# Performance work log

Measured on AMD Instinct MI355X. Metric: run time of the kernel, lower is better.

The kernel has to match this reference:

```python
import jax, jax.numpy as jnp
import numpy as np

N_NODES = 50000
N_EDGES = 800000
D_IN = 128
D_OUT = 128
K = 3


def setup_inputs() -> dict:
    key = jax.random.key(0)
    k1, k2, k3, k4 = jax.random.split(key, 4)
    x = jax.random.normal(k1, (N_NODES, D_IN), dtype=jnp.float32)
    src = jax.random.randint(k2, (N_EDGES,), 0, N_NODES, dtype=jnp.int32)
    dst = jax.random.randint(k3, (N_EDGES,), 0, N_NODES, dtype=jnp.int32)
    edge_index = jnp.stack([src, dst], axis=0)  # [2, E]
    W = jax.random.normal(k4, (D_OUT, D_IN * (K + 1)), dtype=jnp.float32) * 0.02
    b = jnp.zeros((D_OUT,), dtype=jnp.float32)
    return {"x": x, "edge_index": edge_index, "W": W, "b": b}


def _mean_propagate(h, src, dst, n_nodes):
    # scatter-mean: out[v] = mean_{(u,v) in E} h[u]
    msgs = h[src]                                             # [E, D] gather
    summed = jax.ops.segment_sum(msgs, dst, num_segments=n_nodes)
    cnt = jax.ops.segment_sum(jnp.ones((src.shape[0], 1), h.dtype), dst,
                              num_segments=n_nodes)
    return summed / jnp.maximum(cnt, 1.0)


def reference(x, edge_index, W, b):
    src, dst = edge_index[0], edge_index[1]
    n = x.shape[0]
    terms = [x]
    terms.append(_mean_propagate(x, src, dst, n))             # T1 = P x
    for _ in range(K - 1):                                    # T_k = 2 P T_{k-1} - T_{k-2}
        terms.append(2.0 * _mean_propagate(terms[-1], src, dst, n) - terms[-2])
    h = jnp.concatenate(terms, axis=-1)                       # [N, D*(K+1)]
    return h @ W.T + b
```

## Files before the change

### kernel.cpp

```cpp
#include <hip/hip_runtime.h>
#include <stdint.h>

#define D 128
#define LDHB 512
#define MAXD 64
#define FILL_SUB 128

typedef unsigned short u16;
typedef __attribute__((ext_vector_type(8))) short short8;
typedef __attribute__((ext_vector_type(4))) float f32x4;

__device__ __forceinline__ u16 f2bf(float f) {
    uint32_t u = __builtin_bit_cast(uint32_t, f);
    u += 0x7FFFu + ((u >> 16) & 1u);
    return (u16)(u >> 16);
}
__device__ __forceinline__ float bflo(uint32_t w) {
    return __builtin_bit_cast(float, w << 16);
}
__device__ __forceinline__ float bfhi(uint32_t w) {
    return __builtin_bit_cast(float, w & 0xFFFF0000u);
}
__device__ __forceinline__ uint32_t packbf(float lo, float hi) {
    return (uint32_t)f2bf(lo) | ((uint32_t)f2bf(hi) << 16);
}
__device__ __forceinline__ uint32_t sel8(const uint4& a, const uint4& b, int j) {
    switch (j) {
        case 0: return a.x; case 1: return a.y; case 2: return a.z; case 3: return a.w;
        case 4: return b.x; case 5: return b.y; case 6: return b.z; default: return b.w;
    }
}


__global__ void zero_kernel(int* __restrict__ p, int n) {
    int i = blockIdx.x * blockDim.x + threadIdx.x;
    if (i < n) p[i] = 0;
}

__global__ void sentinel_kernel(uint4* __restrict__ ell4, int total4, uint32_t pat) {
    int i = blockIdx.x * blockDim.x + threadIdx.x;
    if (i < total4) ell4[i] = make_uint4(pat, pat, pat, pat);
}

__global__ __launch_bounds__(256) void fill_ell_kernel(
        const int* __restrict__ src, const int* __restrict__ dst, int E, int n,
        int* __restrict__ cnt, u16* __restrict__ ell) {
    int grp = blockIdx.x & 7;
    int sub = blockIdx.x >> 3;
    int S = (n + 7) >> 3;
    int lo = grp * S;
    int hi = lo + S; if (hi > n) hi = n;
    const int stride = FILL_SUB * 256;
    for (int i = sub * 256 + (int)threadIdx.x; i < E; i += stride) {
        int d = dst[i];
        if (d >= lo && d < hi) {
            int pos = atomicAdd(&cnt[d], 1);
            if (pos < MAXD) ell[(size_t)d * MAXD + pos] = (u16)src[i];
        }
    }
}


__global__ __launch_bounds__(256) void castx_kernel(const float* __restrict__ x,
                                                    u16* __restrict__ Hb, int n) {
    int gid = blockIdx.x * 256 + threadIdx.x;
    if (gid >= (n + 1) * 16) return;
    int row = gid >> 4, c8 = (gid & 15) * 8;
    uint4 o;
    if (row < n) {
        const float4* p = (const float4*)(x + (size_t)row * D + c8);
        float4 f0 = p[0], f1 = p[1];
        o.x = packbf(f0.x, f0.y); o.y = packbf(f0.z, f0.w);
        o.z = packbf(f1.x, f1.y); o.w = packbf(f1.z, f1.w);
    } else {
        o = make_uint4(0, 0, 0, 0);
    }
    *(uint4*)(Hb + (size_t)row * LDHB + c8) = o;
}

__global__ void zrow_kernel(u16* __restrict__ Hb, int n) {
    int i = threadIdx.x;
    if (i < 48) ((uint4*)(Hb + (size_t)n * LDHB + 128))[i] = make_uint4(0, 0, 0, 0);
}


__global__ __launch_bounds__(256) void packw_kernel(const float* __restrict__ W,
                                                    u16* __restrict__ Bp) {
    int o = blockIdx.x * 256 + threadIdx.x;
    int kt = o >> 13, rem = o & 8191;
    int j = rem >> 6, w = rem & 63, s2 = w >> 3, e = w & 7;
    int k16 = s2 ^ (j & 7);
    int k = kt * 64 + k16 * 8 + e;
    const float* Wj = W + (size_t)j * 512;
    float val;
    if (k < 128)      val = Wj[k] - Wj[k + 256];
    else if (k < 256) val = Wj[k] - 3.0f * Wj[k + 256];
    else if (k < 384) val = 2.0f * Wj[k];
    else              val = 4.0f * Wj[k];
    Bp[o] = f2bf(val);
}


__global__ __launch_bounds__(256) void prop_kernel(u16* __restrict__ Hb, int colin,
                                                   int colout,
                                                   const int* __restrict__ cnt,
                                                   const u16* __restrict__ ell,
                                                   int np) {
    int g = blockIdx.x * 16 + ((int)threadIdx.x >> 4);
    if (g >= np) return;
    int c8 = ((int)threadIdx.x & 15) * 8;
    int deg = cnt[g];
    if (deg > MAXD) deg = MAXD;
    const u16* row = ell + (size_t)g * MAXD;
    float a0 = 0, a1 = 0, a2 = 0, a3 = 0, a4 = 0, a5 = 0, a6 = 0, a7 = 0;
    for (int base = 0; base < deg; base += 16) {
        uint4 i0 = *(const uint4*)(row + base);
        uint4 i1 = *(const uint4*)(row + base + 8);
#pragma unroll
        for (int j = 0; j < 16; ++j) {
            int s = (int)((sel8(i0, i1, j >> 1) >> ((j & 1) * 16)) & 0xFFFFu);
            uint4 v = *(const uint4*)(Hb + (size_t)s * LDHB + colin + c8);
            a0 += bflo(v.x); a1 += bfhi(v.x);
            a2 += bflo(v.y); a3 += bfhi(v.y);
            a4 += bflo(v.z); a5 += bfhi(v.z);
            a6 += bflo(v.w); a7 += bfhi(v.w);
        }
    }
    float inv = 1.0f / (float)(deg > 1 ? deg : 1);
    uint4 o;
    o.x = packbf(a0 * inv, a1 * inv); o.y = packbf(a2 * inv, a3 * inv);
    o.z = packbf(a4 * inv, a5 * inv); o.w = packbf(a6 * inv, a7 * inv);
    *(uint4*)(Hb + (size_t)g * LDHB + colout + c8) = o;
}


__global__ __launch_bounds__(256) void gemm_kernel(const u16* __restrict__ Hb,
                                                   const u16* __restrict__ Bp,
                                                   const float* __restrict__ bias,
                                                   float* __restrict__ out, int n) {
    __shared__ uint4 Asm[128 * 8];
    __shared__ uint4 Bsm[128 * 8];

    const int t = (int)threadIdx.x;
    const int wave = t >> 6, lane = t & 63;
    const int wr = wave >> 1, wc = wave & 1;
    const int m0 = blockIdx.x * 128;
    const int lrow = lane & 15, lk = lane >> 4;

    f32x4 acc[4][4];
#pragma unroll
    for (int m = 0; m < 4; ++m)
#pragma unroll
        for (int nf = 0; nf < 4; ++nf) acc[m][nf] = (f32x4)0.0f;

#pragma unroll 1
    for (int kt = 0; kt < 8; ++kt) {
#pragma unroll
        for (int i = 0; i < 4; ++i) {
            int flat = i * 256 + t;
            int row = flat >> 3, c16 = flat & 7;
            int grow = m0 + row;
            uint4 v = make_uint4(0, 0, 0, 0);
            if (grow < n) v = *(const uint4*)(Hb + (size_t)grow * LDHB + kt * 64 + c16 * 8);
            Asm[row * 8 + (c16 ^ (row & 7))] = v;
        }
        const u16* bsrc = Bp + kt * 8192;
#pragma unroll
        for (int i = 0; i < 4; ++i) {
            int flat = i * 256 + t;
            Bsm[flat] = *(const uint4*)(bsrc + flat * 8);
        }
        __syncthreads();

#pragma unroll
        for (int kk2 = 0; kk2 < 2; ++kk2) {
            int k16 = kk2 * 4 + lk;
            short8 af[4], bfv[4];
#pragma unroll
            for (int m = 0; m < 4; ++m) {
                int r = wr * 64 + m * 16 + lrow;
                af[m] = __builtin_bit_cast(short8, Asm[r * 8 + (k16 ^ (r & 7))]);
            }
#pragma unroll
            for (int nf = 0; nf < 4; ++nf) {
                int j = wc * 64 + nf * 16 + lrow;
                bfv[nf] = __builtin_bit_cast(short8, Bsm[j * 8 + (k16 ^ (j & 7))]);
            }
#pragma unroll
            for (int m = 0; m < 4; ++m)
#pragma unroll
                for (int nf = 0; nf < 4; ++nf)
                    acc[m][nf] = __builtin_amdgcn_mfma_f32_16x16x32_bf16(
                        af[m], bfv[nf], acc[m][nf], 0, 0, 0);
        }
        __syncthreads();
    }

#pragma unroll
    for (int nf = 0; nf < 4; ++nf) {
        int j = wc * 64 + nf * 16 + lrow;
        float bj = bias[j];
#pragma unroll
        for (int m = 0; m < 4; ++m) {
            int rbase = m0 + wr * 64 + m * 16 + lk * 4;
#pragma unroll
            for (int q = 0; q < 4; ++q) {
                int row = rbase + q;
                if (row < n) out[(size_t)row * D + j] = acc[m][nf][q] + bj;
            }
        }
    }
}


static inline size_t align_up(size_t x, size_t a) { return (x + a - 1) & ~(a - 1); }

extern "C" void kernel_launch(void* const* d_in, const int* in_sizes, int n_in,
                              void* d_out, int out_size, void* d_ws, size_t ws_size,
                              hipStream_t stream) {
    const float* x  = (const float*)d_in[0];
    const int*   ei = (const int*)d_in[1];
    const float* W  = (const float*)d_in[2];
    const float* b  = (const float*)d_in[3];
    float* out = (float*)d_out;

    const int n = in_sizes[0] / D;
    const int E = in_sizes[1] / 2;
    const int* src = ei;
    const int* dst = ei + E;
    const int np = n + 1;

    char* w = (char*)d_ws;
    size_t o = 0;
    int* cnt = (int*)(w + o); o = align_up(o + (size_t)np * 4, 256);
    u16* ell = (u16*)(w + o); o = align_up(o + (size_t)n * MAXD * 2, 256);
    u16* Hb  = (u16*)(w + o); o = align_up(o + (size_t)np * LDHB * 2, 256);
    u16* Bp  = (u16*)(w + o); o = align_up(o + (size_t)65536 * 2, 256);
    (void)ws_size;

    zero_kernel<<<(np + 255) / 256, 256, 0, stream>>>(cnt, np);
    const int total4 = n * MAXD / 8;
    const uint32_t pat = (uint32_t)n | ((uint32_t)n << 16);
    sentinel_kernel<<<(total4 + 255) / 256, 256, 0, stream>>>((uint4*)ell, total4, pat);
    fill_ell_kernel<<<8 * FILL_SUB, 256, 0, stream>>>(src, dst, E, n, cnt, ell);

    castx_kernel<<<(np * 16 + 255) / 256, 256, 0, stream>>>(x, Hb, n);
    zrow_kernel<<<1, 64, 0, stream>>>(Hb, n);
    packw_kernel<<<256, 256, 0, stream>>>(W, Bp);

    const int pgrid = (np + 15) / 16;
    prop_kernel<<<pgrid, 256, 0, stream>>>(Hb, 0,   128, cnt, ell, np);
    prop_kernel<<<pgrid, 256, 0, stream>>>(Hb, 128, 256, cnt, ell, np);
    prop_kernel<<<pgrid, 256, 0, stream>>>(Hb, 256, 384, cnt, ell, np);

    gemm_kernel<<<(n + 127) / 128, 256, 0, stream>>>(Hb, Bp, b, out, n);
}
```

Measured before the change: 235.2 us.

## Merge init kernels, vectorize ELL fill, wave-per-node propagation, smaller GEMM tiles

Fuses the zero and sentinel kernels into one init kernel and folds the zero-row write into the cast kernel, cutting launch count. The ELL fill now reads dst and src as int4 and skips src loads when no edge falls in the block's range, with twice as many sub-blocks. Propagation moves from 16 lanes per node loading uint4 to a full wave per node loading 32-bit words, with neighbor indices broadcast by shuffle. The GEMM tile drops from 128 to 64 rows for more blocks. The fill assumes E is divisible by 4, and the narrower gathers issue more, smaller memory requests.

```diff
diff --git a/kernel.cpp b/kernel.cpp
--- a/kernel.cpp
+++ b/kernel.cpp
@@ -4,7 +4,7 @@
 #define D 128
 #define LDHB 512
 #define MAXD 64
-#define FILL_SUB 128
+#define FILL_SUB 256
 
 typedef unsigned short u16;
 typedef __attribute__((ext_vector_type(8))) short short8;
@@ -24,26 +24,18 @@
 __device__ __forceinline__ uint32_t packbf(float lo, float hi) {
     return (uint32_t)f2bf(lo) | ((uint32_t)f2bf(hi) << 16);
 }
-__device__ __forceinline__ uint32_t sel8(const uint4& a, const uint4& b, int j) {
-    switch (j) {
-        case 0: return a.x; case 1: return a.y; case 2: return a.z; case 3: return a.w;
-        case 4: return b.x; case 5: return b.y; case 6: return b.z; default: return b.w;
-    }
-}
-
-
-__global__ void zero_kernel(int* __restrict__ p, int n) {
-    int i = blockIdx.x * blockDim.x + threadIdx.x;
-    if (i < n) p[i] = 0;
-}
-
-__global__ void sentinel_kernel(uint4* __restrict__ ell4, int total4, uint32_t pat) {
-    int i = blockIdx.x * blockDim.x + threadIdx.x;
+
+
+__global__ __launch_bounds__(256) void init_kernel(int* __restrict__ cnt, int np,
+                                                   uint4* __restrict__ ell4, int total4,
+                                                   uint32_t pat) {
+    int i = blockIdx.x * 256 + threadIdx.x;
+    if (i < np) cnt[i] = 0;
     if (i < total4) ell4[i] = make_uint4(pat, pat, pat, pat);
 }
 
 __global__ __launch_bounds__(256) void fill_ell_kernel(
-        const int* __restrict__ src, const int* __restrict__ dst, int E, int n,
+        const int4* __restrict__ src4, const int4* __restrict__ dst4, int E4, int n,
         int* __restrict__ cnt, u16* __restrict__ ell) {
     int grp = blockIdx.x & 7;
     int sub = blockIdx.x >> 3;
@@ -51,36 +43,43 @@
     int lo = grp * S;
     int hi = lo + S; if (hi > n) hi = n;
     const int stride = FILL_SUB * 256;
-    for (int i = sub * 256 + (int)threadIdx.x; i < E; i += stride) {
-        int d = dst[i];
-        if (d >= lo && d < hi) {
-            int pos = atomicAdd(&cnt[d], 1);
-            if (pos < MAXD) ell[(size_t)d * MAXD + pos] = (u16)src[i];
-        }
+    for (int i = sub * 256 + (int)threadIdx.x; i < E4; i += stride) {
+        int4 d = dst4[i];
+        bool cx = (d.x >= lo) & (d.x < hi);
+        bool cy = (d.y >= lo) & (d.y < hi);
+        bool cz = (d.z >= lo) & (d.z < hi);
+        bool cw = (d.w >= lo) & (d.w < hi);
+        if (!(cx | cy | cz | cw)) continue;
+        int4 s = src4[i];
+        if (cx) { int p = atomicAdd(&cnt[d.x], 1); if (p < MAXD) ell[(size_t)d.x * MAXD + p] = (u16)s.x; }
+        if (cy) { int p = atomicAdd(&cnt[d.y], 1); if (p < MAXD) ell[(size_t)d.y * MAXD + p] = (u16)s.y; }
+        if (cz) { int p = atomicAdd(&cnt[d.z], 1); if (p < MAXD) ell[(size_t)d.z * MAXD + p] = (u16)s.z; }
+        if (cw) { int p = atomicAdd(&cnt[d.w], 1); if (p < MAXD) ell[(size_t)d.w * MAXD + p] = (u16)s.w; }
     }
 }
 
 
 __global__ __launch_bounds__(256) void castx_kernel(const float* __restrict__ x,
                                                     u16* __restrict__ Hb, int n) {
+    int np = n + 1;
     int gid = blockIdx.x * 256 + threadIdx.x;
-    if (gid >= (n + 1) * 16) return;
-    int row = gid >> 4, c8 = (gid & 15) * 8;
-    uint4 o;
-    if (row < n) {
-        const float4* p = (const float4*)(x + (size_t)row * D + c8);
-        float4 f0 = p[0], f1 = p[1];
-        o.x = packbf(f0.x, f0.y); o.y = packbf(f0.z, f0.w);
-        o.z = packbf(f1.x, f1.y); o.w = packbf(f1.z, f1.w);
+    int totalx = np * 16;
+    if (gid < totalx) {
+        int row = gid >> 4, c8 = (gid & 15) * 8;
+        uint4 o;
+        if (row < n) {
+            const float4* p = (const float4*)(x + (size_t)row * D + c8);
+            float4 f0 = p[0], f1 = p[1];
+            o.x = packbf(f0.x, f0.y); o.y = packbf(f0.z, f0.w);
+            o.z = packbf(f1.x, f1.y); o.w = packbf(f1.z, f1.w);
+        } else {
+            o = make_uint4(0, 0, 0, 0);
+        }
+        *(uint4*)(Hb + (size_t)row * LDHB + c8) = o;
     } else {
-        o = make_uint4(0, 0, 0, 0);
-    }
-    *(uint4*)(Hb + (size_t)row * LDHB + c8) = o;
-}
-
-__global__ void zrow_kernel(u16* __restrict__ Hb, int n) {
-    int i = threadIdx.x;
-    if (i < 48) ((uint4*)(Hb + (size_t)n * LDHB + 128))[i] = make_uint4(0, 0, 0, 0);
+        int e = gid - totalx;
+        if (e < 48) ((uint4*)(Hb + (size_t)n * LDHB + 128))[e] = make_uint4(0, 0, 0, 0);
+    }
 }
 
 
@@ -106,31 +105,24 @@
                                                    const int* __restrict__ cnt,
                                                    const u16* __restrict__ ell,
                                                    int np) {
-    int g = blockIdx.x * 16 + ((int)threadIdx.x >> 4);
+    int g = blockIdx.x * 4 + ((int)threadIdx.x >> 6);
     if (g >= np) return;
-    int c8 = ((int)threadIdx.x & 15) * 8;
+    int lane = (int)threadIdx.x & 63;
     int deg = cnt[g];
     if (deg > MAXD) deg = MAXD;
     const u16* row = ell + (size_t)g * MAXD;
-    float a0 = 0, a1 = 0, a2 = 0, a3 = 0, a4 = 0, a5 = 0, a6 = 0, a7 = 0;
+    float alo = 0.f, ahi = 0.f;
     for (int base = 0; base < deg; base += 16) {
-        uint4 i0 = *(const uint4*)(row + base);
-        uint4 i1 = *(const uint4*)(row + base + 8);
+        int si = (int)row[base + (lane & 15)];
 #pragma unroll
         for (int j = 0; j < 16; ++j) {
-            int s = (int)((sel8(i0, i1, j >> 1) >> ((j & 1) * 16)) & 0xFFFFu);
-            uint4 v = *(const uint4*)(Hb + (size_t)s * LDHB + colin + c8);
-            a0 += bflo(v.x); a1 += bfhi(v.x);
-            a2 += bflo(v.y); a3 += bfhi(v.y);
-            a4 += bflo(v.z); a5 += bfhi(v.z);
-            a6 += bflo(v.w); a7 += bfhi(v.w);
+            int s = __shfl(si, j, 16);
+            uint32_t v = *(const uint32_t*)(Hb + (size_t)s * LDHB + colin + lane * 2);
+            alo += bflo(v); ahi += bfhi(v);
         }
     }
     float inv = 1.0f / (float)(deg > 1 ? deg : 1);
-    uint4 o;
-    o.x = packbf(a0 * inv, a1 * inv); o.y = packbf(a2 * inv, a3 * inv);
-    o.z = packbf(a4 * inv, a5 * inv); o.w = packbf(a6 * inv, a7 * inv);
-    *(uint4*)(Hb + (size_t)g * LDHB + colout + c8) = o;
+    *(uint32_t*)(Hb + (size_t)g * LDHB + colout + lane * 2) = packbf(alo * inv, ahi * inv);
 }
 
 
@@ -138,25 +130,25 @@
                                                    const u16* __restrict__ Bp,
                                                    const float* __restrict__ bias,
                                                    float* __restrict__ out, int n) {
-    __shared__ uint4 Asm[128 * 8];
+    __shared__ uint4 Asm[64 * 8];
     __shared__ uint4 Bsm[128 * 8];
 
     const int t = (int)threadIdx.x;
     const int wave = t >> 6, lane = t & 63;
     const int wr = wave >> 1, wc = wave & 1;
-    const int m0 = blockIdx.x * 128;
+    const int m0 = blockIdx.x * 64;
     const int lrow = lane & 15, lk = lane >> 4;
 
-    f32x4 acc[4][4];
-#pragma unroll
-    for (int m = 0; m < 4; ++m)
+    f32x4 acc[2][4];
+#pragma unroll
+    for (int m = 0; m < 2; ++m)
 #pragma unroll
         for (int nf = 0; nf < 4; ++nf) acc[m][nf] = (f32x4)0.0f;
 
 #pragma unroll 1
     for (int kt = 0; kt < 8; ++kt) {
 #pragma unroll
-        for (int i = 0; i < 4; ++i) {
+        for (int i = 0; i < 2; ++i) {
             int flat = i * 256 + t;
             int row = flat >> 3, c16 = flat & 7;
             int grow = m0 + row;
@@ -175,10 +167,10 @@
 #pragma unroll
         for (int kk2 = 0; kk2 < 2; ++kk2) {
             int k16 = kk2 * 4 + lk;
-            short8 af[4], bfv[4];
-#pragma unroll
-            for (int m = 0; m < 4; ++m) {
-                int r = wr * 64 + m * 16 + lrow;
+            short8 af[2], bfv[4];
+#pragma unroll
+            for (int m = 0; m < 2; ++m) {
+                int r = wr * 32 + m * 16 + lrow;
                 af[m] = __builtin_bit_cast(short8, Asm[r * 8 + (k16 ^ (r & 7))]);
             }
 #pragma unroll
@@ -187,7 +179,7 @@
                 bfv[nf] = __builtin_bit_cast(short8, Bsm[j * 8 + (k16 ^ (j & 7))]);
             }
 #pragma unroll
-            for (int m = 0; m < 4; ++m)
+            for (int m = 0; m < 2; ++m)
 #pragma unroll
                 for (int nf = 0; nf < 4; ++nf)
                     acc[m][nf] = __builtin_amdgcn_mfma_f32_16x16x32_bf16(
@@ -201,8 +193,8 @@
         int j = wc * 64 + nf * 16 + lrow;
         float bj = bias[j];
 #pragma unroll
-        for (int m = 0; m < 4; ++m) {
-            int rbase = m0 + wr * 64 + m * 16 + lk * 4;
+        for (int m = 0; m < 2; ++m) {
+            int rbase = m0 + wr * 32 + m * 16 + lk * 4;
 #pragma unroll
             for (int q = 0; q < 4; ++q) {
                 int row = rbase + q;
@@ -238,20 +230,20 @@
     u16* Bp  = (u16*)(w + o); o = align_up(o + (size_t)65536 * 2, 256);
     (void)ws_size;
 
-    zero_kernel<<<(np + 255) / 256, 256, 0, stream>>>(cnt, np);
     const int total4 = n * MAXD / 8;
     const uint32_t pat = (uint32_t)n | ((uint32_t)n << 16);
-    sentinel_kernel<<<(total4 + 255) / 256, 256, 0, stream>>>((uint4*)ell, total4, pat);
-    fill_ell_kernel<<<8 * FILL_SUB, 256, 0, stream>>>(src, dst, E, n, cnt, ell);
-
-    castx_kernel<<<(np * 16 + 255) / 256, 256, 0, stream>>>(x, Hb, n);
-    zrow_kernel<<<1, 64, 0, stream>>>(Hb, n);
+    const int initN = (total4 > np ? total4 : np);
+    init_kernel<<<(initN + 255) / 256, 256, 0, stream>>>(cnt, np, (uint4*)ell, total4, pat);
+    fill_ell_kernel<<<8 * FILL_SUB, 256, 0, stream>>>((const int4*)src, (const int4*)dst,
+                                                      E / 4, n, cnt, ell);
+
+    castx_kernel<<<(np * 16 + 48 + 255) / 256, 256, 0, stream>>>(x, Hb, n);
     packw_kernel<<<256, 256, 0, stream>>>(W, Bp);
 
-    const int pgrid = (np + 15) / 16;
+    const int pgrid = (np + 3) / 4;
     prop_kernel<<<pgrid, 256, 0, stream>>>(Hb, 0,   128, cnt, ell, np);
     prop_kernel<<<pgrid, 256, 0, stream>>>(Hb, 128, 256, cnt, ell, np);
     prop_kernel<<<pgrid, 256, 0, stream>>>(Hb, 256, 384, cnt, ell, np);
 
-    gemm_kernel<<<(n + 127) / 128, 256, 0, stream>>>(Hb, Bp, b, out, n);
-}
+    gemm_kernel<<<(n + 63) / 64, 256, 0, stream>>>(Hb, Bp, b, out, n);
+}
```

Measured after the change: 230.6 us. Within noise of the previous version (-1.9%).
